# Kernel optimization log

Measured on AMD Instinct MI355X. Metric: run time of the kernel, lower is better.

Reference implementation:

```python
import jax, jax.numpy as jnp
import numpy as np

D_MODEL = 1024
EXPAND = 2
INNER = D_MODEL * EXPAND  # 2048
D_STATE = 64
K = 3
BSZ = 2
SEQ = 4096


def setup_inputs() -> dict:
    key = jax.random.key(0)
    ks = jax.random.split(key, 12)
    s = 0.02

    def w(k, shape):
        return jax.random.normal(k, shape, jnp.float32) * s

    return {
        "x": jax.random.normal(ks[0], (BSZ, SEQ, D_MODEL), jnp.float32),
        "W_in": w(ks[1], (D_MODEL, 2 * INNER)),
        "b_in": jnp.zeros((2 * INNER,), jnp.float32),
        "conv_w": w(ks[2], (INNER, K)),            # depthwise kernel per channel
        "conv_b": jnp.zeros((INNER,), jnp.float32),
        "W_dt": w(ks[3], (INNER, D_STATE)),
        "b_dt": jnp.zeros((D_STATE,), jnp.float32),
        "W_B": w(ks[4], (INNER, D_STATE)),
        "b_B": jnp.zeros((D_STATE,), jnp.float32),
        "W_C": w(ks[5], (INNER, D_STATE)),
        "b_C": jnp.zeros((D_STATE,), jnp.float32),
        "W_si": w(ks[6], (D_STATE, INNER)),
        "b_si": jnp.zeros((INNER,), jnp.float32),
        "D": jnp.ones((INNER,), jnp.float32),
        "W_out": w(ks[7], (INNER, D_MODEL)),
        "b_out": jnp.zeros((D_MODEL,), jnp.float32),
    }


def reference(x, W_in, b_in, conv_w, conv_b, W_dt, b_dt, W_B, b_B, W_C, b_C,
              W_si, b_si, D, W_out, b_out):
    bsz, seq_len, _ = x.shape
    inner = W_in.shape[1] // 2
    k = conv_w.shape[1]

    xz = x @ W_in + b_in                      # [B, L, 2*inner]
    x_main, gate = xz[..., :inner], xz[..., inner:]

    # Causal depthwise conv: torch pads k-1 both sides then slices [:L],
    # equivalent to left-pad (k-1), right-pad 0.
    lhs = jnp.transpose(x_main, (0, 2, 1))    # [B, C, L]
    rhs = conv_w[:, None, :]                  # [C, 1, K]
    conv = jax.lax.conv_general_dilated(
        lhs, rhs, window_strides=(1,), padding=[(k - 1, 0)],
        dimension_numbers=("NCH", "OIH", "NCH"), feature_group_count=inner)
    x_main = jnp.transpose(conv, (0, 2, 1)) + conv_b  # [B, L, inner]
    x_main = jax.nn.silu(x_main)

    dt = jax.nn.sigmoid(x_main @ W_dt + b_dt)  # [B, L, d_state]
    Bm = x_main @ W_B + b_B
    Cm = x_main @ W_C + b_C

    # Selective state recurrence: state_t = (1-dt_t)*state_{t-1} + dt_t*B_t
    def step(state, inp):
        dt_t, B_t, C_t = inp                  # each [B, d_state]
        state = (1.0 - dt_t) * state + dt_t * B_t
        return state, C_t * state

    xs = (jnp.moveaxis(dt, 1, 0), jnp.moveaxis(Bm, 1, 0), jnp.moveaxis(Cm, 1, 0))
    state0 = jnp.zeros((bsz, dt.shape[-1]), x.dtype)
    _, y = jax.lax.scan(step, state0, xs)     # [L, B, d_state]
    y = jnp.moveaxis(y, 0, 1)                 # [B, L, d_state]

    # LayerNorm over last dim, no affine, eps=1e-5 (torch F.layer_norm default)
    mu = jnp.mean(y, axis=-1, keepdims=True)
    var = jnp.var(y, axis=-1, keepdims=True)
    y = (y - mu) * jax.lax.rsqrt(var + 1e-5)

    y = y @ W_si + b_si                       # [B, L, inner]
    y = y + D * x_main
    y = y * jax.nn.sigmoid(gate)
    return y @ W_out + b_out                  # [B, L, d_model]
```

## Files before the change

### kernel.cpp

```cpp
#include <hip/hip_runtime.h>
#include <hip/hip_bf16.h>
#include <math.h>


namespace {

typedef __bf16 bf16x8 __attribute__((ext_vector_type(8)));
typedef float  f32x4  __attribute__((ext_vector_type(4)));
typedef unsigned short u16;

constexpr int kSeq = 4096;

__device__ __forceinline__ float sigmoid_f(float x) { return 1.0f / (1.0f + expf(-x)); }
__device__ __forceinline__ u16   f2bf(float f) { __bf16 h = (__bf16)f; return __builtin_bit_cast(u16, h); }
__device__ __forceinline__ float bf2f(u16 u)   { return (float)__builtin_bit_cast(__bf16, u); }

__device__ __forceinline__ void gll16(const u16* g, u16* l) {
    __builtin_amdgcn_global_load_lds(
        (const __attribute__((address_space(1))) unsigned int*)g,
        (__attribute__((address_space(3))) unsigned int*)l,
        16, 0, 0);
}

__device__ __forceinline__ int xcd_swizzle(int lin, int nwg) {
    const int q = nwg >> 3, r = nwg & 7;
    const int xcd = lin & 7, idx = lin >> 3;
    return (xcd < r ? xcd * (q + 1) : r * (q + 1) + (xcd - r) * q) + idx;
}

__global__ __launch_bounds__(256)
void convert_bf16(const float* __restrict__ in, u16* __restrict__ out, long n4)
{
    long i = (long)blockIdx.x * 256 + threadIdx.x;
    if (i >= n4) return;
    float4 v = reinterpret_cast<const float4*>(in)[i];
    ushort4 o = make_ushort4(f2bf(v.x), f2bf(v.y), f2bf(v.z), f2bf(v.w));
    reinterpret_cast<ushort4*>(out)[i] = o;
}

__device__ __forceinline__ void tr_body(float (*tile)[33],
                                        const float* __restrict__ in, u16* __restrict__ out,
                                        int R, int C, int r0, int c0, int t)
{
    const int lr = t >> 3, lc = (t & 7) * 4;
    float4 v = *reinterpret_cast<const float4*>(in + (size_t)(r0 + lr) * C + c0 + lc);
    tile[lr][lc + 0] = v.x; tile[lr][lc + 1] = v.y;
    tile[lr][lc + 2] = v.z; tile[lr][lc + 3] = v.w;
    __syncthreads();
    const int oc = t >> 3, orr = (t & 7) * 4;
    ushort4 o = make_ushort4(f2bf(tile[orr + 0][oc]), f2bf(tile[orr + 1][oc]),
                             f2bf(tile[orr + 2][oc]), f2bf(tile[orr + 3][oc]));
    *reinterpret_cast<ushort4*>(out + (size_t)(c0 + oc) * R + r0 + orr) = o;
}

__global__ __launch_bounds__(256)
void transpose_big(const float* __restrict__ Win, u16* __restrict__ WinT,
                   const float* __restrict__ Wout, u16* __restrict__ WoutT)
{
    __shared__ float tile[32][33];
    const int t = threadIdx.x;
    if (blockIdx.z == 0) {
        tr_body(tile, Win, WinT, 1024, 4096, blockIdx.y * 32, blockIdx.x * 32, t);
    } else {
        if (blockIdx.x >= 64) return;
        tr_body(tile, Wout, WoutT, 2048, 1024, blockIdx.x * 32, blockIdx.y * 32, t);
    }
}

__global__ __launch_bounds__(256)
void transpose_small(const float* __restrict__ Wdt, const float* __restrict__ WB,
                     const float* __restrict__ WC,  const float* __restrict__ Wsi,
                     u16* __restrict__ WdtbcT, u16* __restrict__ WsiT)
{
    __shared__ float tile[32][33];
    const int t = threadIdx.x;
    const int z = blockIdx.z;
    if (z < 3) {
        const float* in = (z == 0) ? Wdt : (z == 1) ? WB : WC;
        u16* out = WdtbcT + (size_t)z * 64 * 2048;
        tr_body(tile, in, out, 2048, 64, blockIdx.y * 32, blockIdx.x * 32, t);
    } else {
        tr_body(tile, Wsi, WsiT, 64, 2048, blockIdx.x * 32, blockIdx.y * 32, t);
    }
}

template <int BM, int BN, int EPI>
__global__ __launch_bounds__(256)
void gemm_mfma(const u16* __restrict__ A, const u16* __restrict__ Bt,
               const float* __restrict__ b0, const float* __restrict__ b1,
               const float* __restrict__ b2,
               const u16* __restrict__ aux0, const u16* __restrict__ aux1,
               void* __restrict__ o0, int N, int K, int nbx)
{
    constexpr int FM = BM / 32, FN = BN / 32;
    constexpr int CA = BM / 32, CB = BN / 32;
    __shared__ __align__(16) u16 As[BM][64];
    __shared__ __align__(16) u16 Bs[BN][64];

    const int tid  = threadIdx.x;
    const int lane = tid & 63;
    const int wid  = tid >> 6;
    const int wr   = (wid >> 1) * (BM / 2);
    const int wc   = (wid & 1)  * (BN / 2);
    const int swz  = xcd_swizzle(blockIdx.x, gridDim.x);
    const int row0 = (swz / nbx) * BM;
    const int col0 = (swz % nbx) * BN;

    const int srow = lane >> 3;
    const int scol = ((lane & 7) ^ srow) * 8;
    const int fr   = lane & 15;
    const int fq   = lane >> 4;

    f32x4 acc[FM][FN];
#pragma unroll
    for (int m = 0; m < FM; ++m)
#pragma unroll
        for (int n = 0; n < FN; ++n) acc[m][n] = (f32x4){0.f, 0.f, 0.f, 0.f};

    for (int k0 = 0; k0 < K; k0 += 64) {
#pragma unroll
        for (int i = 0; i < CA; ++i) {
            const int c = wid * CA + i;
            gll16(A + (size_t)(row0 + c * 8 + srow) * K + k0 + scol,
                  &As[0][0] + c * 512 + lane * 8);
        }
#pragma unroll
        for (int i = 0; i < CB; ++i) {
            const int c = wid * CB + i;
            gll16(Bt + (size_t)(col0 + c * 8 + srow) * K + k0 + scol,
                  &Bs[0][0] + c * 512 + lane * 8);
        }
        __syncthreads();
#pragma unroll
        for (int kk = 0; kk < 2; ++kk) {
            bf16x8 af[FM], bg[FN];
#pragma unroll
            for (int m = 0; m < FM; ++m) {
                const int rr = wr + m * 16 + fr;
                af[m] = *reinterpret_cast<const bf16x8*>(
                    &As[rr][(kk * 32 + fq * 8) ^ ((rr & 7) * 8)]);
            }
#pragma unroll
            for (int n = 0; n < FN; ++n) {
                const int rr = wc + n * 16 + fr;
                bg[n] = *reinterpret_cast<const bf16x8*>(
                    &Bs[rr][(kk * 32 + fq * 8) ^ ((rr & 7) * 8)]);
            }
#pragma unroll
            for (int m = 0; m < FM; ++m)
#pragma unroll
                for (int n = 0; n < FN; ++n)
                    acc[m][n] = __builtin_amdgcn_mfma_f32_16x16x32_bf16(af[m], bg[n], acc[m][n], 0, 0, 0);
        }
        __syncthreads();
    }

#pragma unroll
    for (int m = 0; m < FM; ++m) {
#pragma unroll
        for (int n = 0; n < FN; ++n) {
            const int gc  = col0 + wc + n * 16 + fr;
            const int gr0 = row0 + wr + m * 16 + fq * 4;
            if constexpr (EPI == 2) {
                float4 vv;
                float* vp = (float*)&vv;
#pragma unroll
                for (int j = 0; j < 4; ++j) {
                    float bb = (gc < 64) ? b0[gc] : (gc < 128) ? b1[gc - 64] : b2[gc - 128];
                    float v = acc[m][n][j] + bb;
                    if (gc < 64) v = sigmoid_f(v);
                    vp[j] = v;
                }
                *reinterpret_cast<float4*>(&((float*)o0)[(size_t)gc * 8192 + gr0]) = vv;
            } else {
#pragma unroll
                for (int j = 0; j < 4; ++j) {
                    const int gr = gr0 + j;
                    float v = acc[m][n][j];
                    if constexpr (EPI == 0) {
                        ((float*)o0)[(size_t)gr * N + gc] = v + b0[gc];
                    } else if constexpr (EPI == 1) {
                        ((u16*)o0)[(size_t)gr * N + gc] = f2bf(v + b0[gc]);
                    } else {
                        const size_t p = (size_t)gr * 2048 + gc;
                        float g  = bf2f(aux0[(size_t)gr * 4096 + gc]);
                        float xa = bf2f(aux1[p]);
                        v = v + b0[gc] + b1[gc] * xa;
                        ((u16*)o0)[p] = f2bf(v * sigmoid_f(g));
                    }
                }
            }
        }
    }
    (void)b1; (void)b2; (void)aux0; (void)aux1;
}

__global__ __launch_bounds__(256)
void conv_silu(const u16* __restrict__ xz, const float* __restrict__ cw,
               const float* __restrict__ cb, u16* __restrict__ xact)
{
    const size_t g  = ((size_t)blockIdx.x * 256 + threadIdx.x) * 8;
    const int    c0 = (int)(g & 2047);
    const size_t r  = g >> 11;
    const int    s  = (int)(r & (kSeq - 1));
    const u16* p = xz + r * 4096 + c0;
    u16 X0[8], X1[8] = {}, X2[8] = {};
    *reinterpret_cast<uint4*>(X0) = *reinterpret_cast<const uint4*>(p);
    if (s >= 1) *reinterpret_cast<uint4*>(X1) = *reinterpret_cast<const uint4*>(p - 4096);
    if (s >= 2) *reinterpret_cast<uint4*>(X2) = *reinterpret_cast<const uint4*>(p - 8192);
    u16 O[8];
#pragma unroll
    for (int j = 0; j < 8; ++j) {
        const int c = c0 + j;
        float v = bf2f(X2[j]) * cw[c * 3 + 0] + bf2f(X1[j]) * cw[c * 3 + 1]
                + bf2f(X0[j]) * cw[c * 3 + 2] + cb[c];
        O[j] = f2bf(v * sigmoid_f(v));
    }
    *reinterpret_cast<uint4*>(xact + r * 2048 + c0) = *reinterpret_cast<uint4*>(O);
}

__global__ __launch_bounds__(256)
void scan_kernel(const float* __restrict__ dtbcT, float* __restrict__ y)
{
    const int b = blockIdx.x >> 6;
    const int d = blockIdx.x & 63;
    const int t = threadIdx.x;
    const size_t col = (size_t)b * kSeq + t * 16;
    const float* dtp = dtbcT + (size_t)d         * 8192 + col;
    const float* Bp  = dtbcT + (size_t)(64 + d)  * 8192 + col;
    const float* Cp  = dtbcT + (size_t)(128 + d) * 8192 + col;

    float av[16], bv[16];
    float Acc = 1.f, Bcc = 0.f;
#pragma unroll
    for (int q = 0; q < 4; ++q) {
        float4 dv = *reinterpret_cast<const float4*>(dtp + q * 4);
        float4 Bv = *reinterpret_cast<const float4*>(Bp + q * 4);
        const float* dvp = (const float*)&dv;
        const float* bvp = (const float*)&Bv;
#pragma unroll
        for (int j = 0; j < 4; ++j) {
            const int i = q * 4 + j;
            float a  = 1.f - dvp[j];
            float bb = dvp[j] * bvp[j];
            av[i] = a; bv[i] = bb;
            Acc = a * Acc;
            Bcc = a * Bcc + bb;
        }
    }

    __shared__ float sA[256], sB[256];
    sA[t] = Acc; sB[t] = Bcc;
    __syncthreads();
    for (int off = 1; off < 256; off <<= 1) {
        float cA = sA[t], cB = sB[t];
        float pA = 1.f, pB = 0.f;
        if (t >= off) { pA = sA[t - off]; pB = sB[t - off]; }
        __syncthreads();
        if (t >= off) { sA[t] = cA * pA; sB[t] = cA * pB + cB; }
        __syncthreads();
    }

    float s = (t == 0) ? 0.f : sB[t - 1];
#pragma unroll
    for (int q = 0; q < 4; ++q) {
        float4 Cv = *reinterpret_cast<const float4*>(Cp + q * 4);
        const float* cvp = (const float*)&Cv;
#pragma unroll
        for (int j = 0; j < 4; ++j) {
            const int i = q * 4 + j;
            s = av[i] * s + bv[i];
            y[(col + i) * 64 + d] = cvp[j] * s;
        }
    }
}

__global__ __launch_bounds__(256)
void ln_kernel(const float* __restrict__ y, u16* __restrict__ ynb)
{
    const int w = threadIdx.x >> 6;
    const int l = threadIdx.x & 63;
    const size_t r = (size_t)blockIdx.x * 4 + w;
    float v  = y[r * 64 + l];
    float s  = v, s2 = v * v;
#pragma unroll
    for (int m = 1; m < 64; m <<= 1) {
        s  += __shfl_xor(s, m, 64);
        s2 += __shfl_xor(s2, m, 64);
    }
    float mu  = s * (1.f / 64.f);
    float var = s2 * (1.f / 64.f) - mu * mu;
    ynb[r * 64 + l] = f2bf((v - mu) * rsqrtf(var + 1e-5f));
}

}

extern "C" void kernel_launch(void* const* d_in, const int* in_sizes, int n_in,
                              void* d_out, int out_size, void* d_ws, size_t ws_size,
                              hipStream_t stream)
{
    (void)in_sizes; (void)n_in; (void)out_size; (void)ws_size;
    const float* x     = (const float*)d_in[0];
    const float* W_in  = (const float*)d_in[1];
    const float* b_in  = (const float*)d_in[2];
    const float* cw    = (const float*)d_in[3];
    const float* cb    = (const float*)d_in[4];
    const float* W_dt  = (const float*)d_in[5];
    const float* b_dt  = (const float*)d_in[6];
    const float* W_B   = (const float*)d_in[7];
    const float* b_B   = (const float*)d_in[8];
    const float* W_C   = (const float*)d_in[9];
    const float* b_C   = (const float*)d_in[10];
    const float* W_si  = (const float*)d_in[11];
    const float* b_si  = (const float*)d_in[12];
    const float* Dv    = (const float*)d_in[13];
    const float* W_out = (const float*)d_in[14];
    const float* b_out = (const float*)d_in[15];
    float* out = (float*)d_out;

    char* ws = (char*)d_ws;
    u16*   xzb    = (u16*)  (ws);
    u16*   xb     = (u16*)  (ws + 67108864);
    u16*   xact   = (u16*)  (ws + 83886080);
    u16*   hb     = (u16*)  (ws + 117440512);
    float* dtbcT  = (float*)(ws + 150994944);
    float* ybuf   = (float*)(ws + 157286400);
    u16*   ynb    = (u16*)  (ws + 159383552);
    u16*   WinT   = (u16*)  (ws + 160432128);
    u16*   WoutT  = (u16*)  (ws + 168820736);
    u16*   WdtbcT = (u16*)  (ws + 173015040);
    u16*   WsiT   = (u16*)  (ws + 173801472);

    dim3 blk(256);

    convert_bf16<<<dim3((8192L * 1024 / 4 + 255) / 256), blk, 0, stream>>>(x, xb, 8192L * 1024 / 4);
    transpose_big<<<dim3(128, 32, 2), blk, 0, stream>>>(W_in, WinT, W_out, WoutT);
    transpose_small<<<dim3(2, 64, 4), blk, 0, stream>>>(W_dt, W_B, W_C, W_si, WdtbcT, WsiT);

    gemm_mfma<128, 128, 1><<<dim3(32 * 64), blk, 0, stream>>>(
        xb, WinT, b_in, nullptr, nullptr, nullptr, nullptr, xzb, 4096, 1024, 32);
    conv_silu<<<dim3(8192L * 2048 / (8 * 256)), blk, 0, stream>>>(xzb, cw, cb, xact);
    gemm_mfma<64, 64, 2><<<dim3(3 * 128), blk, 0, stream>>>(
        xact, WdtbcT, b_dt, b_B, b_C, nullptr, nullptr, dtbcT, 192, 2048, 3);
    scan_kernel<<<dim3(128), blk, 0, stream>>>(dtbcT, ybuf);
    ln_kernel<<<dim3(8192 / 4), blk, 0, stream>>>(ybuf, ynb);
    gemm_mfma<128, 128, 3><<<dim3(16 * 64), blk, 0, stream>>>(
        ynb, WsiT, b_si, Dv, nullptr, xzb + 2048, xact, hb, 2048, 64, 16);
    gemm_mfma<128, 128, 0><<<dim3(8 * 64), blk, 0, stream>>>(
        hb, WoutT, b_out, nullptr, nullptr, nullptr, nullptr, out, 1024, 2048, 8);
}
```

Baseline: 237.8 us.

## Add 256-row 8-wave GEMM kernel, widen projection tile, and use wave-shuffle scan

Adds a new 512-thread GEMM with 256-row tiles, double-buffered direct-to-LDS loads, XOR-swizzled LDS, and interleaved barrier/priority scheduling. It replaces the input and output projection GEMMs with this kernel to raise data reuse per tile. The dt/B/C projection now uses a single 64x192 tile per row block instead of three 64x64 column tiles. The scan's block-level prefix now uses wave shuffles plus a small cross-wave combine instead of a shared-memory Hillis-Steele loop with many barriers. The trade-off is higher register and LDS pressure in the large GEMM and only 128 blocks for the projection GEMM.

Result: slower. 275.6 us (+15.9%).

```diff
diff --git a/kernel.cpp b/kernel.cpp
--- a/kernel.cpp
+++ b/kernel.cpp
@@ -84,6 +84,150 @@
     }
 }
 
+#define READ_A(MH)                                                        \
+    _Pragma("unroll")                                                     \
+    for (int m = 0; m < 4; ++m) {                                         \
+        const int rb = (((MH) * 4 + m) * 16 + fr) * 64;                   \
+        _Pragma("unroll")                                                 \
+        for (int kk = 0; kk < 2; ++kk)                                    \
+            af[m][kk] = *reinterpret_cast<const bf16x8*>(                 \
+                &As[cur][wrow][0] + rb + (((kk * 4 + fq) * 8) ^ frx));    \
+    }
+
+#define READ_B(DST, NH)                                                   \
+    _Pragma("unroll")                                                     \
+    for (int n = 0; n < FNH; ++n) {                                       \
+        const int rb = (rbB + ((NH) * FNH + n) * 16 + fr) * 64;           \
+        _Pragma("unroll")                                                 \
+        for (int kk = 0; kk < 2; ++kk)                                    \
+            DST[n][kk] = *reinterpret_cast<const bf16x8*>(                \
+                &Bs[cur][hb][0] + rb + (((kk * 4 + fq) * 8) ^ frx));      \
+    }
+
+#define MMAQ(MH, NH, BG)                                                  \
+    __builtin_amdgcn_s_setprio(1);                                        \
+    _Pragma("unroll")                                                     \
+    for (int m = 0; m < 4; ++m)                                           \
+        _Pragma("unroll")                                                 \
+        for (int n = 0; n < FNH; ++n)                                     \
+            _Pragma("unroll")                                             \
+            for (int kk = 0; kk < 2; ++kk)                                \
+                acc[(MH) * 4 + m][(NH) * FNH + n] =                       \
+                    __builtin_amdgcn_mfma_f32_16x16x32_bf16(              \
+                        af[m][kk], BG[n][kk],                             \
+                        acc[(MH) * 4 + m][(NH) * FNH + n], 0, 0, 0);      \
+    __builtin_amdgcn_s_setprio(0);
+
+template <int BN, int EPI>
+__global__ __launch_bounds__(512, 2)
+void gemm256(const u16* __restrict__ A, const u16* __restrict__ Bt,
+             const float* __restrict__ b0, void* __restrict__ o0,
+             int N, int K, int nbx)
+{
+    constexpr int FN  = BN / 64;
+    constexpr int FNH = FN / 2;
+    constexpr int NB  = BN / 128;
+    constexpr int HSZ = 128 * 64;
+
+    __shared__ __align__(16) u16 As[2][2][HSZ];
+    __shared__ __align__(16) u16 Bs[2][NB][HSZ];
+
+    const int tid  = threadIdx.x;
+    const int lane = tid & 63;
+    const int wid  = tid >> 6;
+    const int wrow = wid >> 2;
+    const int wcol = wid & 3;
+    const int swz  = xcd_swizzle(blockIdx.x, gridDim.x);
+    const int row0 = (swz / nbx) * 256;
+    const int col0 = (swz % nbx) * BN;
+
+    const int srow = lane >> 3;
+    const int scol = ((lane & 7) ^ srow) * 8;
+    const int fr   = lane & 15;
+    const int fq   = lane >> 4;
+    const int frx  = (fr & 7) * 8;
+    const int nt   = K / 64;
+
+    const int hb  = (NB == 2) ? (wcol >> 1) : 0;
+    const int rbB = (NB == 2) ? ((wcol & 1) * 64) : (wcol * 32);
+
+    auto stageA = [&](int u, int h) {
+        u16* dst = &As[u & 1][h][0] + wid * 1024 + lane * 8;
+        const u16* src = A + (size_t)(row0 + h * 128 + wid * 16 + srow) * K + u * 64 + scol;
+        gll16(src, dst);
+        gll16(src + (size_t)8 * K, dst + 512);
+    };
+    auto stageB = [&](int u, int h) {
+        u16* dst = &Bs[u & 1][h][0] + wid * 1024 + lane * 8;
+        const u16* src = Bt + (size_t)(col0 + h * 128 + wid * 16 + srow) * K + u * 64 + scol;
+        gll16(src, dst);
+        gll16(src + (size_t)8 * K, dst + 512);
+    };
+
+    f32x4 acc[8][FN];
+#pragma unroll
+    for (int m = 0; m < 8; ++m)
+#pragma unroll
+        for (int n = 0; n < FN; ++n) acc[m][n] = (f32x4){0.f, 0.f, 0.f, 0.f};
+
+    stageA(0, 0); stageB(0, 0);
+    if (NB == 2) stageB(0, 1);
+    stageA(0, 1);
+    if (nt > 1) { stageB(1, 0); stageA(1, 0); }
+    if (nt > 1) asm volatile("s_waitcnt vmcnt(4)" ::: "memory");
+    else        asm volatile("s_waitcnt vmcnt(0)" ::: "memory");
+    __builtin_amdgcn_s_barrier();
+
+    bf16x8 af[4][2], bg0[FNH][2], bg1[FNH][2];
+
+    for (int u = 0; u < nt; ++u) {
+        const int cur = u & 1;
+        if (u + 1 < nt) stageA(u + 1, 1);
+        READ_A(0)
+        READ_B(bg0, 0)
+        __builtin_amdgcn_s_barrier();
+        MMAQ(0, 0, bg0)
+        __builtin_amdgcn_s_barrier();
+        if (NB == 2 && u + 1 < nt) stageB(u + 1, 1);
+        READ_B(bg1, 1)
+        __builtin_amdgcn_s_barrier();
+        MMAQ(0, 1, bg1)
+        __builtin_amdgcn_s_barrier();
+        if (u + 2 < nt) stageB(u + 2, 0);
+        READ_A(1)
+        __builtin_amdgcn_s_barrier();
+        MMAQ(1, 1, bg1)
+        __builtin_amdgcn_s_barrier();
+        if (u + 2 < nt) stageA(u + 2, 0);
+        __builtin_amdgcn_s_barrier();
+        MMAQ(1, 0, bg0)
+        if (u + 2 < nt) asm volatile("s_waitcnt vmcnt(4)" ::: "memory");
+        else            asm volatile("s_waitcnt vmcnt(0)" ::: "memory");
+        __builtin_amdgcn_s_barrier();
+    }
+
+#pragma unroll
+    for (int m = 0; m < 8; ++m) {
+#pragma unroll
+        for (int n = 0; n < FN; ++n) {
+            const int gc  = col0 + wcol * (BN / 4) + n * 16 + fr;
+            const int gr0 = row0 + wrow * 128 + m * 16 + fq * 4;
+#pragma unroll
+            for (int j = 0; j < 4; ++j) {
+                const float v = acc[m][n][j] + b0[gc];
+                if constexpr (EPI == 0) {
+                    ((float*)o0)[(size_t)(gr0 + j) * N + gc] = v;
+                } else {
+                    ((u16*)o0)[(size_t)(gr0 + j) * N + gc] = f2bf(v);
+                }
+            }
+        }
+    }
+}
+#undef READ_A
+#undef READ_B
+#undef MMAQ
+
 template <int BM, int BN, int EPI>
 __global__ __launch_bounds__(256)
 void gemm_mfma(const u16* __restrict__ A, const u16* __restrict__ Bt,
@@ -176,18 +320,11 @@
 #pragma unroll
                 for (int j = 0; j < 4; ++j) {
                     const int gr = gr0 + j;
-                    float v = acc[m][n][j];
-                    if constexpr (EPI == 0) {
-                        ((float*)o0)[(size_t)gr * N + gc] = v + b0[gc];
-                    } else if constexpr (EPI == 1) {
-                        ((u16*)o0)[(size_t)gr * N + gc] = f2bf(v + b0[gc]);
-                    } else {
-                        const size_t p = (size_t)gr * 2048 + gc;
-                        float g  = bf2f(aux0[(size_t)gr * 4096 + gc]);
-                        float xa = bf2f(aux1[p]);
-                        v = v + b0[gc] + b1[gc] * xa;
-                        ((u16*)o0)[p] = f2bf(v * sigmoid_f(g));
-                    }
+                    const size_t p = (size_t)gr * 2048 + gc;
+                    float g  = bf2f(aux0[(size_t)gr * 4096 + gc]);
+                    float xa = bf2f(aux1[p]);
+                    float v = acc[m][n][j] + b0[gc] + b1[gc] * xa;
+                    ((u16*)o0)[p] = f2bf(v * sigmoid_f(g));
                 }
             }
         }
@@ -225,6 +362,8 @@
     const int b = blockIdx.x >> 6;
     const int d = blockIdx.x & 63;
     const int t = threadIdx.x;
+    const int lane = t & 63;
+    const int w = t >> 6;
     const size_t col = (size_t)b * kSeq + t * 16;
     const float* dtp = dtbcT + (size_t)d         * 8192 + col;
     const float* Bp  = dtbcT + (size_t)(64 + d)  * 8192 + col;
@@ -249,19 +388,22 @@
         }
     }
 
-    __shared__ float sA[256], sB[256];
-    sA[t] = Acc; sB[t] = Bcc;
+#pragma unroll
+    for (int off = 1; off < 64; off <<= 1) {
+        float pA = __shfl_up(Acc, off, 64);
+        float pB = __shfl_up(Bcc, off, 64);
+        if (lane >= off) { Bcc = Acc * pB + Bcc; Acc = Acc * pA; }
+    }
+    __shared__ float wA[4], wB[4];
+    if (lane == 63) { wA[w] = Acc; wB[w] = Bcc; }
+    float eA = __shfl_up(Acc, 1, 64);
+    float eB = __shfl_up(Bcc, 1, 64);
+    if (lane == 0) { eA = 1.f; eB = 0.f; }
     __syncthreads();
-    for (int off = 1; off < 256; off <<= 1) {
-        float cA = sA[t], cB = sB[t];
-        float pA = 1.f, pB = 0.f;
-        if (t >= off) { pA = sA[t - off]; pB = sB[t - off]; }
-        __syncthreads();
-        if (t >= off) { sA[t] = cA * pA; sB[t] = cA * pB + cB; }
-        __syncthreads();
-    }
-
-    float s = (t == 0) ? 0.f : sB[t - 1];
+    float sW = 0.f;
+    for (int i = 0; i < w; ++i) sW = wA[i] * sW + wB[i];
+    float s = eA * sW + eB;
+
 #pragma unroll
     for (int q = 0; q < 4; ++q) {
         float4 Cv = *reinterpret_cast<const float4*>(Cp + q * 4);
@@ -332,20 +474,21 @@
     u16*   WsiT   = (u16*)  (ws + 173801472);
 
     dim3 blk(256);
+    dim3 blk512(512);
 
     convert_bf16<<<dim3((8192L * 1024 / 4 + 255) / 256), blk, 0, stream>>>(x, xb, 8192L * 1024 / 4);
     transpose_big<<<dim3(128, 32, 2), blk, 0, stream>>>(W_in, WinT, W_out, WoutT);
     transpose_small<<<dim3(2, 64, 4), blk, 0, stream>>>(W_dt, W_B, W_C, W_si, WdtbcT, WsiT);
 
-    gemm_mfma<128, 128, 1><<<dim3(32 * 64), blk, 0, stream>>>(
-        xb, WinT, b_in, nullptr, nullptr, nullptr, nullptr, xzb, 4096, 1024, 32);
+    gemm256<256, 1><<<dim3(32 * 16), blk512, 0, stream>>>(
+        xb, WinT, b_in, xzb, 4096, 1024, 16);
     conv_silu<<<dim3(8192L * 2048 / (8 * 256)), blk, 0, stream>>>(xzb, cw, cb, xact);
-    gemm_mfma<64, 64, 2><<<dim3(3 * 128), blk, 0, stream>>>(
-        xact, WdtbcT, b_dt, b_B, b_C, nullptr, nullptr, dtbcT, 192, 2048, 3);
+    gemm_mfma<64, 192, 2><<<dim3(128), blk, 0, stream>>>(
+        xact, WdtbcT, b_dt, b_B, b_C, nullptr, nullptr, dtbcT, 192, 2048, 1);
     scan_kernel<<<dim3(128), blk, 0, stream>>>(dtbcT, ybuf);
     ln_kernel<<<dim3(8192 / 4), blk, 0, stream>>>(ybuf, ynb);
     gemm_mfma<128, 128, 3><<<dim3(16 * 64), blk, 0, stream>>>(
         ynb, WsiT, b_si, Dv, nullptr, xzb + 2048, xact, hb, 2048, 64, 16);
-    gemm_mfma<128, 128, 0><<<dim3(8 * 64), blk, 0, stream>>>(
-        hb, WoutT, b_out, nullptr, nullptr, nullptr, nullptr, out, 1024, 2048, 8);
-}
+    gemm256<128, 0><<<dim3(32 * 8), blk512, 0, stream>>>(
+        hb, WoutT, b_out, out, 1024, 2048, 8);
+}
```
